# Performance work log

Measured on AMD Instinct MI355X. Metric: run time of the kernel, lower is better.

Reference implementation:

```python
import jax, jax.numpy as jnp
import numpy as np
from jax import lax

T, B, IN, H = 512, 64, 1024, 1024
N_LAYER = 2


def _kaiming_uniform(key, shape):
    # torch kaiming_uniform_ default: a=sqrt(5) -> gain = sqrt(2/(1+5)) = 1/sqrt(3)
    fan_in = shape[1]
    gain = 1.0 / np.sqrt(3.0)
    bound = gain * np.sqrt(3.0 / fan_in)
    return jax.random.uniform(key, shape, jnp.float32, -bound, bound)


def setup_inputs() -> dict:
    key = jax.random.key(0)
    ks = jax.random.split(key, 5)
    inputs = jax.random.normal(ks[0], (T, B, IN), jnp.float32)
    # layer 0: input_size -> hidden; layer 1: hidden -> hidden
    w_ih0 = _kaiming_uniform(ks[1], (4 * H, IN))
    w_hh0 = _kaiming_uniform(ks[2], (4 * H, H))
    b0 = jnp.zeros((4 * H,), jnp.float32)
    w_ih1 = _kaiming_uniform(ks[3], (4 * H, H))
    w_hh1 = _kaiming_uniform(ks[4], (4 * H, H))
    b1 = jnp.zeros((4 * H,), jnp.float32)
    return {"inputs": inputs, "w_ih0": w_ih0, "w_hh0": w_hh0, "b0": b0,
            "w_ih1": w_ih1, "w_hh1": w_hh1, "b1": b1}


def _lstm_layer(x_seq, w_ih, w_hh, b):
    # x_seq: [T, B, D]; initial h = ones (per source hx=None branch), c = zeros
    batch = x_seq.shape[1]
    hidden = w_hh.shape[1]
    h0 = jnp.ones((batch, hidden), x_seq.dtype)
    c0 = jnp.zeros((batch, hidden), x_seq.dtype)

    def step(carry, x_t):
        h, c = carry
        gates = x_t @ w_ih.T + h @ w_hh.T + b  # [B, 4H]
        i, f, g, o = jnp.split(gates, 4, axis=-1)
        i = jax.nn.sigmoid(i)
        f = jax.nn.sigmoid(f)
        g = jnp.tanh(g)
        o = jax.nn.sigmoid(o)
        c_new = f * c + i * g
        h_new = o * jnp.tanh(c_new)
        return (h_new, c_new), h_new

    _, hs = lax.scan(step, (h0, c0), x_seq)
    return hs  # [T, B, H]


def reference(inputs, w_ih0, w_hh0, b0, w_ih1, w_hh1, b1):
    h1 = _lstm_layer(inputs, w_ih0, w_hh0, b0)
    h2 = _lstm_layer(h1, w_ih1, w_hh1, b1)
    return h2  # [T, B, H]
```

## Files before the change

kernel.cpp:

```cpp
#include <hip/hip_runtime.h>
#include <cstdint>
#include <cstddef>


typedef _Float16 f16;
typedef _Float16 f16x8 __attribute__((ext_vector_type(8)));
typedef _Float16 f16x4 __attribute__((ext_vector_type(4)));
typedef float    f32x4 __attribute__((ext_vector_type(4)));
typedef unsigned long long u64;

#define T_STEPS 512
#define BH      65536
#define NBLK    256

static const size_t OFF_FLAG = 0;
static const size_t OFF_H2   = 0x1000;
static const size_t OFF_H1   = 0x90000;

__global__ void prep_kernel(f16* __restrict__ h1, unsigned* __restrict__ flags)
{
    const int NONES = BH / 4;
    const int NZ    = NBLK / 4;
    int tid    = blockIdx.x * blockDim.x + threadIdx.x;
    int stride = gridDim.x * blockDim.x;
    f16x4 one = { (f16)1.f, (f16)1.f, (f16)1.f, (f16)1.f };
    uint4 z = { 0u, 0u, 0u, 0u };
    for (int i = tid; i < NONES + NZ; i += stride) {
        if (i < NONES) ((f16x4*)h1)[i] = one;
        else           ((uint4*)flags)[i - NONES] = z;
    }
}

__device__ __forceinline__ float sigm(float x) { return 1.f/(1.f + __expf(-x)); }
__device__ __forceinline__ float tanh_f(float x) {
    float e = __expf(-2.f*fabsf(x));
    float r = (1.f - e)/(1.f + e);
    return x >= 0.f ? r : -r;
}
__device__ __forceinline__ f16x8 cvt8(float4 a, float4 b) {
    f16x8 r;
    r[0]=(f16)a.x; r[1]=(f16)a.y; r[2]=(f16)a.z; r[3]=(f16)a.w;
    r[4]=(f16)b.x; r[5]=(f16)b.y; r[6]=(f16)b.z; r[7]=(f16)b.w;
    return r;
}

__device__ __forceinline__ unsigned poll1(const unsigned* p) {
    unsigned r;
    asm volatile("global_load_dword %0, %1, off sc1\n\ts_waitcnt vmcnt(0)"
                 : "=v"(r) : "v"(p) : "memory");
    return r;
}
__device__ __forceinline__ uint2 poll2(const unsigned* p) {
    uint2 r;
    asm volatile("global_load_dwordx2 %0, %1, off sc1\n\ts_waitcnt vmcnt(0)"
                 : "=v"(r) : "v"(p) : "memory");
    return r;
}
__device__ __forceinline__ void flag_store(unsigned* p, unsigned v) {
    asm volatile("global_store_dword %0, %1, off sc1" :: "v"(p), "v"(v) : "memory");
}
__device__ __forceinline__ f16x8 ald16(const f16* p) {
    union { u64 q[2]; f16x8 v; } u;
    u.q[0] = __hip_atomic_load((const u64*)p,       __ATOMIC_RELAXED, __HIP_MEMORY_SCOPE_AGENT);
    u.q[1] = __hip_atomic_load((const u64*)(p + 4), __ATOMIC_RELAXED, __HIP_MEMORY_SCOPE_AGENT);
    return u.v;
}

__global__ __launch_bounds__(512, 2)
void lstm_kernel(const float* __restrict__ x,
                 const float* __restrict__ wih0, const float* __restrict__ whh0,
                 const float* __restrict__ b0,
                 const float* __restrict__ wih1, const float* __restrict__ whh1,
                 const float* __restrict__ b1,
                 f16* __restrict__ h1, f16* __restrict__ h2,
                 float* __restrict__ out, unsigned* __restrict__ flags)
{
    __shared__ float lds_part[16384];
    __shared__ float lds_out[2048];

    const int tid   = threadIdx.x;
    const int bid   = blockIdx.x;
    const int layer = bid >> 7;
    const int wave  = tid >> 6, lane = tid & 63;
    const int l15   = lane & 15, l4 = lane >> 4;

    f16x8 Bf[32];
    f32x4 acc[8];
    const f32x4 zz = { 0.f, 0.f, 0.f, 0.f };

    if (layer == 0) {
        const int bg = bid >> 6, jg = bid & 63, j0 = jg << 4;
        const int kq = wave;

        {
            const float* wsrc = (kq < 4) ? wih0 : whh0;
            const int kp = (kq & 3) * 256;
#pragma unroll
            for (int nt = 0; nt < 4; nt++) {
                const float* rp = wsrc + (size_t)(nt*1024 + j0 + l15)*1024 + kp + l4*8;
#pragma unroll
                for (int kc = 0; kc < 8; kc++) {
                    float4 a = *(const float4*)(rp + kc*32);
                    float4 b = *(const float4*)(rp + kc*32 + 4);
                    Bf[nt*8 + kc] = cvt8(a, b);
                }
            }
#pragma unroll
            for (int i = 0; i < 32; i++) asm volatile("" : "+v"(Bf[i]));
        }

        const int u  = ((tid >> 8) << 3) | (tid & 7);
        const int bm = (tid >> 3) & 31;
        const float bi  = b0[j0+u],      bff = b0[1024+j0+u];
        const float bgg = b0[2048+j0+u], boo = b0[3072+j0+u];
        float c = 0.f;
        const int m_ = bm >> 4, r_ = bm & 15;
        const int lanei = ((r_ >> 2) << 4) | u, rr = r_ & 3;

        for (int s = 0; s <= T_STEPS; s++) {
            const bool act = (s < T_STEPS);
            if (act) {
#pragma unroll
                for (int i = 0; i < 8; i++) acc[i] = zz;
                if (kq < 4) {
                    const float* a0 = x + (size_t)s*BH + (size_t)(bg*32 + l15)*1024 + kq*256 + l4*8;
                    const float* a1 = a0 + 16*1024;
#pragma unroll
                    for (int kc = 0; kc < 8; kc++) {
                        f16x8 A0 = cvt8(*(const float4*)(a0 + kc*32), *(const float4*)(a0 + kc*32 + 4));
                        f16x8 A1 = cvt8(*(const float4*)(a1 + kc*32), *(const float4*)(a1 + kc*32 + 4));
#pragma unroll
                        for (int nt = 0; nt < 4; nt++) {
                            acc[nt]   = __builtin_amdgcn_mfma_f32_16x16x32_f16(A0, Bf[nt*8+kc], acc[nt],   0,0,0);
                            acc[4+nt] = __builtin_amdgcn_mfma_f32_16x16x32_f16(A1, Bf[nt*8+kc], acc[4+nt], 0,0,0);
                        }
                    }
                } else {
                    if (s > 0) {
                        const unsigned* p = flags + bg*64 + lane;
                        const bool skip = (lane == jg);
                        for (;;) {
                            unsigned v = poll1(p);
                            if (__all(skip || (v >= (unsigned)s))) break;
                            __builtin_amdgcn_s_sleep(2);
                        }
                    }
                    const f16* a0 = h1 + (size_t)s*BH + bg*32768 + ((kq-4)*32 + l4)*256 + l15*8;
                    const f16* a1 = a0 + 128;
#pragma unroll
                    for (int kc = 0; kc < 8; kc++) {
                        f16x8 A0 = *(const f16x8*)(a0 + kc*1024);
                        f16x8 A1 = *(const f16x8*)(a1 + kc*1024);
#pragma unroll
                        for (int nt = 0; nt < 4; nt++) {
                            acc[nt]   = __builtin_amdgcn_mfma_f32_16x16x32_f16(A0, Bf[nt*8+kc], acc[nt],   0,0,0);
                            acc[4+nt] = __builtin_amdgcn_mfma_f32_16x16x32_f16(A1, Bf[nt*8+kc], acc[4+nt], 0,0,0);
                        }
                    }
                }
                const int pb = wave*2048 + lane*4;
#pragma unroll
                for (int i = 0; i < 8; i++)
                    *(f32x4*)&lds_part[pb + i*256] = acc[i];
            }
            __syncthreads();
            if (act) {
                f32x4 sum = *(const f32x4*)&lds_part[tid*4];
#pragma unroll
                for (int q = 1; q < 8; q++)
                    sum += *(const f32x4*)&lds_part[q*2048 + tid*4];
                *(f32x4*)&lds_out[tid*4] = sum;
            }
            __syncthreads();
            if (act) {
                float gi = lds_out[(m_*4+0)*256 + lanei*4 + rr] + bi;
                float gf = lds_out[(m_*4+1)*256 + lanei*4 + rr] + bff;
                float gg = lds_out[(m_*4+2)*256 + lanei*4 + rr] + bgg;
                float go = lds_out[(m_*4+3)*256 + lanei*4 + rr] + boo;
                float iv = sigm(gi), fv = sigm(gf), gv = tanh_f(gg), ov = sigm(go);
                c = fv*c + iv*gv;
                float h = ov * tanh_f(c);
                f16 hv = (f16)h;
                short hs = __builtin_bit_cast(short, hv);
                __hip_atomic_store((short*)(h1 + (size_t)(s+1)*BH + bg*32768 + jg*512 + tid),
                                   hs, __ATOMIC_RELAXED, __HIP_MEMORY_SCOPE_AGENT);
            }
            __builtin_amdgcn_s_waitcnt(0);
            __syncthreads();
            if (tid == 0) flag_store(flags + bid, (unsigned)(s + 1));
        }
    } else {
        const int jg1 = bid & 127, j0 = jg1 << 3;
        const int kq = wave >> 1, mh = wave & 1;
        const int kp = (kq & 1) * 512;
        {
            const float* wsrc = (kq < 2) ? wih1 : whh1;
#pragma unroll
            for (int nt = 0; nt < 2; nt++) {
                int ln = (nt << 4) + l15;
                int srcrow = (ln >> 3)*1024 + j0 + (ln & 7);
                const float* rp = wsrc + (size_t)srcrow*1024 + kp + l4*8;
#pragma unroll
                for (int kc = 0; kc < 16; kc++) {
                    float4 a = *(const float4*)(rp + kc*32);
                    float4 b = *(const float4*)(rp + kc*32 + 4);
                    Bf[nt*16 + kc] = cvt8(a, b);
                }
            }
#pragma unroll
            for (int i = 0; i < 32; i++) asm volatile("" : "+v"(Bf[i]));
        }

        const int bm = tid >> 3, u = tid & 7, j = j0 + u;
        const float bi = b1[j], bff = b1[1024+j], bgg = b1[2048+j], boo = b1[3072+j];
        float c = 0.f;
        const int li = ((bm >> 2) & 3) << 4, rr = bm & 3, tI = (bm >> 4) << 1;

        for (int s = 0; s <= T_STEPS; s++) {
            const bool act = (s >= 1);
            if (act) {
#pragma unroll
                for (int i = 0; i < 4; i++) acc[i] = zz;
                if (kq < 2) {
                    {
                        const unsigned* p = flags + lane*2;
                        for (;;) {
                            uint2 v = poll2(p);
                            if (__all((v.x >= (unsigned)s) && (v.y >= (unsigned)s))) break;
                            __builtin_amdgcn_s_sleep(2);
                        }
                    }
                    const f16* a0 = h1 + (size_t)s*BH + mh*32768 + (kq*64 + l4)*256 + l15*8;
                    const f16* a1 = a0 + 128;
#pragma unroll
                    for (int kc = 0; kc < 16; kc++) {
                        f16x8 A0 = *(const f16x8*)(a0 + kc*1024);
                        f16x8 A1 = *(const f16x8*)(a1 + kc*1024);
                        acc[0] = __builtin_amdgcn_mfma_f32_16x16x32_f16(A0, Bf[kc],    acc[0], 0,0,0);
                        acc[1] = __builtin_amdgcn_mfma_f32_16x16x32_f16(A0, Bf[16+kc], acc[1], 0,0,0);
                        acc[2] = __builtin_amdgcn_mfma_f32_16x16x32_f16(A1, Bf[kc],    acc[2], 0,0,0);
                        acc[3] = __builtin_amdgcn_mfma_f32_16x16x32_f16(A1, Bf[16+kc], acc[3], 0,0,0);
                    }
                } else if (s == 1) {
                    f16x8 A1s;
#pragma unroll
                    for (int e = 0; e < 8; e++) A1s[e] = (f16)1.f;
#pragma unroll
                    for (int kc = 0; kc < 16; kc++) {
                        acc[0] = __builtin_amdgcn_mfma_f32_16x16x32_f16(A1s, Bf[kc],    acc[0], 0,0,0);
                        acc[1] = __builtin_amdgcn_mfma_f32_16x16x32_f16(A1s, Bf[16+kc], acc[1], 0,0,0);
                        acc[2] = __builtin_amdgcn_mfma_f32_16x16x32_f16(A1s, Bf[kc],    acc[2], 0,0,0);
                        acc[3] = __builtin_amdgcn_mfma_f32_16x16x32_f16(A1s, Bf[16+kc], acc[3], 0,0,0);
                    }
                } else {
                    {
                        const unsigned* p = flags + 128 + lane*2;
                        const bool skip0 = (128 + lane*2     == bid);
                        const bool skip1 = (128 + lane*2 + 1 == bid);
                        for (;;) {
                            uint2 v = poll2(p);
                            if (__all((skip0 || v.x >= (unsigned)s) &&
                                      (skip1 || v.y >= (unsigned)s))) break;
                            __builtin_amdgcn_s_sleep(2);
                        }
                    }
                    const int kq2 = kq - 2;
                    const f16* h2s = h2 + (size_t)((s-1) & 3)*BH;
                    const f16* a0 = h2s + (kq2*64 + l4)*512 + (mh*32 + l15)*8;
                    const f16* a1 = a0 + 128;
#pragma unroll
                    for (int kc = 0; kc < 16; kc++) {
                        f16x8 A0 = ald16(a0 + kc*2048);
                        f16x8 A1 = ald16(a1 + kc*2048);
                        acc[0] = __builtin_amdgcn_mfma_f32_16x16x32_f16(A0, Bf[kc],    acc[0], 0,0,0);
                        acc[1] = __builtin_amdgcn_mfma_f32_16x16x32_f16(A0, Bf[16+kc], acc[1], 0,0,0);
                        acc[2] = __builtin_amdgcn_mfma_f32_16x16x32_f16(A1, Bf[kc],    acc[2], 0,0,0);
                        acc[3] = __builtin_amdgcn_mfma_f32_16x16x32_f16(A1, Bf[16+kc], acc[3], 0,0,0);
                    }
                }
                const int base = kq*2048 + lane*4;
                *(f32x4*)&lds_part[base + ((mh*2+0)*2 + 0)*256] = acc[0];
                *(f32x4*)&lds_part[base + ((mh*2+0)*2 + 1)*256] = acc[1];
                *(f32x4*)&lds_part[base + ((mh*2+1)*2 + 0)*256] = acc[2];
                *(f32x4*)&lds_part[base + ((mh*2+1)*2 + 1)*256] = acc[3];
            }
            __syncthreads();
            if (act) {
                f32x4 sum = *(const f32x4*)&lds_part[tid*4];
                sum += *(const f32x4*)&lds_part[2048 + tid*4];
                sum += *(const f32x4*)&lds_part[4096 + tid*4];
                sum += *(const f32x4*)&lds_part[6144 + tid*4];
                *(f32x4*)&lds_out[tid*4] = sum;
            }
            __syncthreads();
            if (act) {
                float gi = lds_out[(tI+0)*256 + (li +     u)*4 + rr] + bi;
                float gf = lds_out[(tI+0)*256 + (li + 8 + u)*4 + rr] + bff;
                float gg = lds_out[(tI+1)*256 + (li +     u)*4 + rr] + bgg;
                float go = lds_out[(tI+1)*256 + (li + 8 + u)*4 + rr] + boo;
                float iv = sigm(gi), fv = sigm(gf), gv = tanh_f(gg), ov = sigm(go);
                c = fv*c + iv*gv;
                float h = ov * tanh_f(c);
                f16 hv = (f16)h;
                short hs = __builtin_bit_cast(short, hv);
                __hip_atomic_store((short*)(h2 + (size_t)(s & 3)*BH + jg1*512 + tid),
                                   hs, __ATOMIC_RELAXED, __HIP_MEMORY_SCOPE_AGENT);
                out[(size_t)(s-1)*BH + bm*1024 + j] = h;
            }
            __builtin_amdgcn_s_waitcnt(0);
            __syncthreads();
            if (tid == 0) flag_store(flags + bid, (unsigned)(s + 1));
        }
    }
}

extern "C" void kernel_launch(void* const* d_in, const int* in_sizes, int n_in,
                              void* d_out, int out_size, void* d_ws, size_t ws_size,
                              hipStream_t stream) {
    const float* x    = (const float*)d_in[0];
    const float* wih0 = (const float*)d_in[1];
    const float* whh0 = (const float*)d_in[2];
    const float* b0   = (const float*)d_in[3];
    const float* wih1 = (const float*)d_in[4];
    const float* whh1 = (const float*)d_in[5];
    const float* b1   = (const float*)d_in[6];
    float* out = (float*)d_out;

    char* ws = (char*)d_ws;
    unsigned* flags = (unsigned*)(ws + OFF_FLAG);
    f16* h2         = (f16*)(ws + OFF_H2);
    f16* h1         = (f16*)(ws + OFF_H1);

    prep_kernel<<<256, 256, 0, stream>>>(h1, flags);
    lstm_kernel<<<NBLK, 512, 0, stream>>>(x, wih0, whh0, b0, wih1, whh1, b1,
                                          h1, h2, out, flags);
}
```

Measured before the change: 5.214 ms.

## Shrink layer-1 to 64 blocks each covering 16 hidden units and full batch

```diff
diff --git a/kernel.cpp b/kernel.cpp
--- a/kernel.cpp
+++ b/kernel.cpp
@@ -11,7 +11,7 @@
 
 #define T_STEPS 512
 #define BH      65536
-#define NBLK    256
+#define NBLK    192
 
 static const size_t OFF_FLAG = 0;
 static const size_t OFF_H2   = 0x1000;
@@ -20,7 +20,7 @@
 __global__ void prep_kernel(f16* __restrict__ h1, unsigned* __restrict__ flags)
 {
     const int NONES = BH / 4;
-    const int NZ    = NBLK / 4;
+    const int NZ    = 256 / 4;
     int tid    = blockIdx.x * blockDim.x + threadIdx.x;
     int stride = gridDim.x * blockDim.x;
     f16x4 one = { (f16)1.f, (f16)1.f, (f16)1.f, (f16)1.f };
@@ -47,12 +47,6 @@
 __device__ __forceinline__ unsigned poll1(const unsigned* p) {
     unsigned r;
     asm volatile("global_load_dword %0, %1, off sc1\n\ts_waitcnt vmcnt(0)"
-                 : "=v"(r) : "v"(p) : "memory");
-    return r;
-}
-__device__ __forceinline__ uint2 poll2(const unsigned* p) {
-    uint2 r;
-    asm volatile("global_load_dwordx2 %0, %1, off sc1\n\ts_waitcnt vmcnt(0)"
                  : "=v"(r) : "v"(p) : "memory");
     return r;
 }
@@ -75,23 +69,21 @@
                  f16* __restrict__ h1, f16* __restrict__ h2,
                  float* __restrict__ out, unsigned* __restrict__ flags)
 {
-    __shared__ float lds_part[16384];
-    __shared__ float lds_out[2048];
+    __shared__ float lds_part[32768];
+    __shared__ float lds_out[4096];
 
     const int tid   = threadIdx.x;
     const int bid   = blockIdx.x;
-    const int layer = bid >> 7;
     const int wave  = tid >> 6, lane = tid & 63;
     const int l15   = lane & 15, l4 = lane >> 4;
-
-    f16x8 Bf[32];
-    f32x4 acc[8];
     const f32x4 zz = { 0.f, 0.f, 0.f, 0.f };
 
-    if (layer == 0) {
+    if (bid < 128) {
         const int bg = bid >> 6, jg = bid & 63, j0 = jg << 4;
         const int kq = wave;
 
+        f16x8 Bf[32];
+        f32x4 acc[8];
         {
             const float* wsrc = (kq < 4) ? wih0 : whh0;
             const int kp = (kq & 3) * 256;
@@ -137,8 +129,10 @@
                     }
                 } else {
                     if (s > 0) {
-                        const unsigned* p = flags + bg*64 + lane;
-                        const bool skip = (lane == jg);
+                        const bool mine = (lane < 16);
+                        const int  pj   = ((kq - 4) << 4) + l15;
+                        const bool skip = (!mine) || (pj == jg);
+                        const unsigned* p = flags + bg*64 + (mine ? pj : 0);
                         for (;;) {
                             unsigned v = poll1(p);
                             if (__all(skip || (v >= (unsigned)s))) break;
@@ -190,122 +184,149 @@
             if (tid == 0) flag_store(flags + bid, (unsigned)(s + 1));
         }
     } else {
-        const int jg1 = bid & 127, j0 = jg1 << 3;
-        const int kq = wave >> 1, mh = wave & 1;
-        const int kp = (kq & 1) * 512;
+        const int jg1 = bid - 128, j0 = jg1 << 4;
+        const int ks = wave;
+
+        f16x8 Bf[32];
+        f32x4 acc[16];
         {
-            const float* wsrc = (kq < 2) ? wih1 : whh1;
-#pragma unroll
-            for (int nt = 0; nt < 2; nt++) {
-                int ln = (nt << 4) + l15;
-                int srcrow = (ln >> 3)*1024 + j0 + (ln & 7);
-                const float* rp = wsrc + (size_t)srcrow*1024 + kp + l4*8;
-#pragma unroll
-                for (int kc = 0; kc < 16; kc++) {
+            const float* wsrc = (ks < 4) ? wih1 : whh1;
+            const int kp = (ks & 3) * 256;
+#pragma unroll
+            for (int nt = 0; nt < 4; nt++) {
+                const float* rp = wsrc + (size_t)(nt*1024 + j0 + l15)*1024 + kp + l4*8;
+#pragma unroll
+                for (int kc = 0; kc < 8; kc++) {
                     float4 a = *(const float4*)(rp + kc*32);
                     float4 b = *(const float4*)(rp + kc*32 + 4);
-                    Bf[nt*16 + kc] = cvt8(a, b);
+                    Bf[nt*8 + kc] = cvt8(a, b);
                 }
             }
 #pragma unroll
             for (int i = 0; i < 32; i++) asm volatile("" : "+v"(Bf[i]));
         }
 
-        const int bm = tid >> 3, u = tid & 7, j = j0 + u;
-        const float bi = b1[j], bff = b1[1024+j], bgg = b1[2048+j], boo = b1[3072+j];
-        float c = 0.f;
-        const int li = ((bm >> 2) & 3) << 4, rr = bm & 3, tI = (bm >> 4) << 1;
+        const int bb = tid >> 3, u0 = tid & 7, u1 = 8 + u0;
+        const float bi0 = b1[j0+u0], bf0 = b1[1024+j0+u0], bg0v = b1[2048+j0+u0], bo0 = b1[3072+j0+u0];
+        const float bi1 = b1[j0+u1], bf1 = b1[1024+j0+u1], bg1v = b1[2048+j0+u1], bo1 = b1[3072+j0+u1];
+        float c0 = 0.f, c1 = 0.f;
+        const int mt_ = bb >> 4, r_ = bb & 15, rr = r_ & 3, lb = (r_ >> 2) << 4;
 
         for (int s = 0; s <= T_STEPS; s++) {
             const bool act = (s >= 1);
             if (act) {
 #pragma unroll
-                for (int i = 0; i < 4; i++) acc[i] = zz;
-                if (kq < 2) {
+                for (int i = 0; i < 16; i++) acc[i] = zz;
+                if (ks < 4) {
                     {
-                        const unsigned* p = flags + lane*2;
+                        const bool mine = (lane < 32);
+                        const int  pidx = ((lane >> 4) * 64) + (ks << 4) + l15;
+                        const unsigned* p = flags + (mine ? pidx : 0);
                         for (;;) {
-                            uint2 v = poll2(p);
-                            if (__all((v.x >= (unsigned)s) && (v.y >= (unsigned)s))) break;
+                            unsigned v = poll1(p);
+                            if (__all(!mine || (v >= (unsigned)s))) break;
                             __builtin_amdgcn_s_sleep(2);
                         }
                     }
-                    const f16* a0 = h1 + (size_t)s*BH + mh*32768 + (kq*64 + l4)*256 + l15*8;
-                    const f16* a1 = a0 + 128;
-#pragma unroll
-                    for (int kc = 0; kc < 16; kc++) {
+                    const f16* a0 = h1 + (size_t)s*BH + (ks*32 + l4)*256 + l15*8;
+#pragma unroll
+                    for (int kc = 0; kc < 8; kc++) {
                         f16x8 A0 = *(const f16x8*)(a0 + kc*1024);
-                        f16x8 A1 = *(const f16x8*)(a1 + kc*1024);
-                        acc[0] = __builtin_amdgcn_mfma_f32_16x16x32_f16(A0, Bf[kc],    acc[0], 0,0,0);
-                        acc[1] = __builtin_amdgcn_mfma_f32_16x16x32_f16(A0, Bf[16+kc], acc[1], 0,0,0);
-                        acc[2] = __builtin_amdgcn_mfma_f32_16x16x32_f16(A1, Bf[kc],    acc[2], 0,0,0);
-                        acc[3] = __builtin_amdgcn_mfma_f32_16x16x32_f16(A1, Bf[16+kc], acc[3], 0,0,0);
+                        f16x8 A1 = *(const f16x8*)(a0 + kc*1024 + 128);
+                        f16x8 A2 = *(const f16x8*)(a0 + kc*1024 + 32768);
+                        f16x8 A3 = *(const f16x8*)(a0 + kc*1024 + 32768 + 128);
+#pragma unroll
+                        for (int nt = 0; nt < 4; nt++) {
+                            acc[nt]    = __builtin_amdgcn_mfma_f32_16x16x32_f16(A0, Bf[nt*8+kc], acc[nt],    0,0,0);
+                            acc[4+nt]  = __builtin_amdgcn_mfma_f32_16x16x32_f16(A1, Bf[nt*8+kc], acc[4+nt],  0,0,0);
+                            acc[8+nt]  = __builtin_amdgcn_mfma_f32_16x16x32_f16(A2, Bf[nt*8+kc], acc[8+nt],  0,0,0);
+                            acc[12+nt] = __builtin_amdgcn_mfma_f32_16x16x32_f16(A3, Bf[nt*8+kc], acc[12+nt], 0,0,0);
+                        }
                     }
                 } else if (s == 1) {
                     f16x8 A1s;
 #pragma unroll
                     for (int e = 0; e < 8; e++) A1s[e] = (f16)1.f;
 #pragma unroll
-                    for (int kc = 0; kc < 16; kc++) {
-                        acc[0] = __builtin_amdgcn_mfma_f32_16x16x32_f16(A1s, Bf[kc],    acc[0], 0,0,0);
-                        acc[1] = __builtin_amdgcn_mfma_f32_16x16x32_f16(A1s, Bf[16+kc], acc[1], 0,0,0);
-                        acc[2] = __builtin_amdgcn_mfma_f32_16x16x32_f16(A1s, Bf[kc],    acc[2], 0,0,0);
-                        acc[3] = __builtin_amdgcn_mfma_f32_16x16x32_f16(A1s, Bf[16+kc], acc[3], 0,0,0);
+                    for (int kc = 0; kc < 8; kc++) {
+#pragma unroll
+                        for (int nt = 0; nt < 4; nt++) {
+                            acc[nt]    = __builtin_amdgcn_mfma_f32_16x16x32_f16(A1s, Bf[nt*8+kc], acc[nt],    0,0,0);
+                            acc[4+nt]  = __builtin_amdgcn_mfma_f32_16x16x32_f16(A1s, Bf[nt*8+kc], acc[4+nt],  0,0,0);
+                            acc[8+nt]  = __builtin_amdgcn_mfma_f32_16x16x32_f16(A1s, Bf[nt*8+kc], acc[8+nt],  0,0,0);
+                            acc[12+nt] = __builtin_amdgcn_mfma_f32_16x16x32_f16(A1s, Bf[nt*8+kc], acc[12+nt], 0,0,0);
+                        }
                     }
                 } else {
                     {
-                        const unsigned* p = flags + 128 + lane*2;
-                        const bool skip0 = (128 + lane*2     == bid);
-                        const bool skip1 = (128 + lane*2 + 1 == bid);
+                        const bool mine = (lane < 16);
+                        const int  pj   = ((ks - 4) << 4) + l15;
+                        const bool skip = (!mine) || (pj == jg1);
+                        const unsigned* p = flags + 128 + (mine ? pj : 0);
                         for (;;) {
-                            uint2 v = poll2(p);
-                            if (__all((skip0 || v.x >= (unsigned)s) &&
-                                      (skip1 || v.y >= (unsigned)s))) break;
+                            unsigned v = poll1(p);
+                            if (__all(skip || (v >= (unsigned)s))) break;
                             __builtin_amdgcn_s_sleep(2);
                         }
                     }
-                    const int kq2 = kq - 2;
-                    const f16* h2s = h2 + (size_t)((s-1) & 3)*BH;
-                    const f16* a0 = h2s + (kq2*64 + l4)*512 + (mh*32 + l15)*8;
-                    const f16* a1 = a0 + 128;
-#pragma unroll
-                    for (int kc = 0; kc < 16; kc++) {
+                    const f16* a0 = h2 + (size_t)((s-1) & 3)*BH + ((ks-4)*32 + l4)*512 + l15*8;
+#pragma unroll
+                    for (int kc = 0; kc < 8; kc++) {
                         f16x8 A0 = ald16(a0 + kc*2048);
-                        f16x8 A1 = ald16(a1 + kc*2048);
-                        acc[0] = __builtin_amdgcn_mfma_f32_16x16x32_f16(A0, Bf[kc],    acc[0], 0,0,0);
-                        acc[1] = __builtin_amdgcn_mfma_f32_16x16x32_f16(A0, Bf[16+kc], acc[1], 0,0,0);
-                        acc[2] = __builtin_amdgcn_mfma_f32_16x16x32_f16(A1, Bf[kc],    acc[2], 0,0,0);
-                        acc[3] = __builtin_amdgcn_mfma_f32_16x16x32_f16(A1, Bf[16+kc], acc[3], 0,0,0);
-                    }
-                }
-                const int base = kq*2048 + lane*4;
-                *(f32x4*)&lds_part[base + ((mh*2+0)*2 + 0)*256] = acc[0];
-                *(f32x4*)&lds_part[base + ((mh*2+0)*2 + 1)*256] = acc[1];
-                *(f32x4*)&lds_part[base + ((mh*2+1)*2 + 0)*256] = acc[2];
-                *(f32x4*)&lds_part[base + ((mh*2+1)*2 + 1)*256] = acc[3];
-            }
-            __syncthreads();
-            if (act) {
-                f32x4 sum = *(const f32x4*)&lds_part[tid*4];
-                sum += *(const f32x4*)&lds_part[2048 + tid*4];
-                sum += *(const f32x4*)&lds_part[4096 + tid*4];
-                sum += *(const f32x4*)&lds_part[6144 + tid*4];
-                *(f32x4*)&lds_out[tid*4] = sum;
-            }
-            __syncthreads();
-            if (act) {
-                float gi = lds_out[(tI+0)*256 + (li +     u)*4 + rr] + bi;
-                float gf = lds_out[(tI+0)*256 + (li + 8 + u)*4 + rr] + bff;
-                float gg = lds_out[(tI+1)*256 + (li +     u)*4 + rr] + bgg;
-                float go = lds_out[(tI+1)*256 + (li + 8 + u)*4 + rr] + boo;
-                float iv = sigm(gi), fv = sigm(gf), gv = tanh_f(gg), ov = sigm(go);
-                c = fv*c + iv*gv;
-                float h = ov * tanh_f(c);
-                f16 hv = (f16)h;
-                short hs = __builtin_bit_cast(short, hv);
-                __hip_atomic_store((short*)(h2 + (size_t)(s & 3)*BH + jg1*512 + tid),
-                                   hs, __ATOMIC_RELAXED, __HIP_MEMORY_SCOPE_AGENT);
-                out[(size_t)(s-1)*BH + bm*1024 + j] = h;
+                        f16x8 A1 = ald16(a0 + kc*2048 + 128);
+                        f16x8 A2 = ald16(a0 + kc*2048 + 256);
+                        f16x8 A3 = ald16(a0 + kc*2048 + 384);
+#pragma unroll
+                        for (int nt = 0; nt < 4; nt++) {
+                            acc[nt]    = __builtin_amdgcn_mfma_f32_16x16x32_f16(A0, Bf[nt*8+kc], acc[nt],    0,0,0);
+                            acc[4+nt]  = __builtin_amdgcn_mfma_f32_16x16x32_f16(A1, Bf[nt*8+kc], acc[4+nt],  0,0,0);
+                            acc[8+nt]  = __builtin_amdgcn_mfma_f32_16x16x32_f16(A2, Bf[nt*8+kc], acc[8+nt],  0,0,0);
+                            acc[12+nt] = __builtin_amdgcn_mfma_f32_16x16x32_f16(A3, Bf[nt*8+kc], acc[12+nt], 0,0,0);
+                        }
+                    }
+                }
+                const int pb = ks*4096 + lane*4;
+#pragma unroll
+                for (int i = 0; i < 16; i++)
+                    *(f32x4*)&lds_part[pb + i*256] = acc[i];
+            }
+            __syncthreads();
+            if (act) {
+#pragma unroll
+                for (int g = 0; g < 2; g++) {
+                    const int gi_ = tid + g*512;
+                    f32x4 sum = *(const f32x4*)&lds_part[gi_*4];
+#pragma unroll
+                    for (int q = 1; q < 8; q++)
+                        sum += *(const f32x4*)&lds_part[q*4096 + gi_*4];
+                    *(f32x4*)&lds_out[gi_*4] = sum;
+                }
+            }
+            __syncthreads();
+            if (act) {
+                float gi0 = lds_out[(mt_*4+0)*256 + (lb+u0)*4 + rr] + bi0;
+                float gf0 = lds_out[(mt_*4+1)*256 + (lb+u0)*4 + rr] + bf0;
+                float gg0 = lds_out[(mt_*4+2)*256 + (lb+u0)*4 + rr] + bg0v;
+                float go0 = lds_out[(mt_*4+3)*256 + (lb+u0)*4 + rr] + bo0;
+                float gi1 = lds_out[(mt_*4+0)*256 + (lb+u1)*4 + rr] + bi1;
+                float gf1 = lds_out[(mt_*4+1)*256 + (lb+u1)*4 + rr] + bf1;
+                float gg1 = lds_out[(mt_*4+2)*256 + (lb+u1)*4 + rr] + bg1v;
+                float go1 = lds_out[(mt_*4+3)*256 + (lb+u1)*4 + rr] + bo1;
+                float iv0 = sigm(gi0), fv0 = sigm(gf0), gv0 = tanh_f(gg0), ov0 = sigm(go0);
+                float iv1 = sigm(gi1), fv1 = sigm(gf1), gv1 = tanh_f(gg1), ov1 = sigm(go1);
+                c0 = fv0*c0 + iv0*gv0;
+                c1 = fv1*c1 + iv1*gv1;
+                float hv0 = ov0 * tanh_f(c0);
+                float hv1 = ov1 * tanh_f(c1);
+                f16* h2w = h2 + (size_t)(s & 3)*BH;
+                short hs0 = __builtin_bit_cast(short, (f16)hv0);
+                short hs1 = __builtin_bit_cast(short, (f16)hv1);
+                __hip_atomic_store((short*)(h2w + jg1*1024 + tid),       hs0,
+                                   __ATOMIC_RELAXED, __HIP_MEMORY_SCOPE_AGENT);
+                __hip_atomic_store((short*)(h2w + jg1*1024 + 512 + tid), hs1,
+                                   __ATOMIC_RELAXED, __HIP_MEMORY_SCOPE_AGENT);
+                out[(size_t)(s-1)*BH + bb*1024 + j0 + u0] = hv0;
+                out[(size_t)(s-1)*BH + bb*1024 + j0 + u1] = hv1;
             }
             __builtin_amdgcn_s_waitcnt(0);
             __syncthreads();
```

Result: faster. 4.889 ms (-6.2%).
